# Optimization experiments

Hardware: AMD Instinct MI355X
Metric: run time of the kernel (lower is better)

Reference implementation:

```python
import jax, jax.numpy as jnp
import numpy as np

# WikiText-103 adaptive softmax config
CUTOFFS = (0, 20000, 40000, 200000, 267735)  # cluster boundaries


def setup_inputs() -> dict:
    key = jax.random.key(0)
    ks = jax.random.split(key, 12)
    N, D = 1024, 1024
    rn = lambda k, shape, std: jax.random.normal(k, shape, jnp.float32) * std
    return {
        "hidden": jax.random.normal(ks[0], (N, D), jnp.float32),
        "target": jax.random.randint(ks[1], (N,), 0, CUTOFFS[-1], jnp.int32),
        "head_w": rn(ks[2], (20000, 1024), 0.02),
        "head_b": jnp.zeros((20000,), jnp.float32),
        "cluster_w": rn(ks[3], (3, 1024), 0.02),
        "cluster_b": jnp.zeros((3,), jnp.float32),
        "proj0": rn(ks[4], (1024, 1024), 0.01),
        "proj1": rn(ks[5], (1024, 256), 0.01),
        "proj2": rn(ks[6], (1024, 64), 0.01),
        "proj3": rn(ks[7], (1024, 16), 0.01),
        "w1": rn(ks[8], (20000, 256), 0.02),
        "b1": jnp.zeros((20000,), jnp.float32),
        "w2": rn(ks[9], (160000, 64), 0.02),
        "b2": jnp.zeros((160000,), jnp.float32),
        "w3": rn(ks[10], (67735, 16), 0.02),
        "b3": jnp.zeros((67735,), jnp.float32),
    }


def _logit(h, w, b, proj):
    # F.linear(F.linear(h, proj.t()), w, b) == (h @ proj) @ w.T + b
    return (h @ proj) @ w.T + b


def reference(hidden, target, head_w, head_b, cluster_w, cluster_b,
              proj0, proj1, proj2, proj3, w1, b1, w2, b2, w3, b3):
    # head: shortlist vocab (20000) + 3 cluster logits -> [N, 20003]
    hw = jnp.concatenate([head_w, cluster_w], axis=0)
    hb = jnp.concatenate([head_b, cluster_b], axis=0)
    head_lp = jax.nn.log_softmax(_logit(hidden, hw, hb, proj0), axis=-1)

    # cluster 0 (shortlist): logprob directly from head
    t0 = jnp.clip(target, 0, CUTOFFS[1] - 1)
    lp = jnp.take_along_axis(head_lp, t0[:, None].astype(jnp.int32), axis=1)[:, 0]

    tails = [(w1, b1, proj1), (w2, b2, proj2), (w3, b3, proj3)]
    for i, (w, b, p) in enumerate(tails, start=1):
        l, r = CUTOFFS[i], CUTOFFS[i + 1]
        mask = (target >= l) & (target < r)
        ti = jnp.clip(target - l, 0, r - l - 1)
        tail_lp = jax.nn.log_softmax(_logit(hidden, w, b, p), axis=-1)  # [N, r-l]
        # note: torch code indexes head_logprob[:, -i] (reversed cluster order quirk)
        lpi = head_lp[:, -i] + jnp.take_along_axis(tail_lp, ti[:, None], axis=1)[:, 0]
        lp = jnp.where(mask, lpi, lp)

    return -lp  # nll per token, keep_order semantics
```

## Files before the change

### kernel.cpp

```cpp
#include <hip/hip_runtime.h>
#include <math.h>

typedef __bf16 bf16;
typedef __bf16 bf16x4 __attribute__((ext_vector_type(4)));
typedef __bf16 bf16x8 __attribute__((ext_vector_type(8)));
typedef float  f32x4  __attribute__((ext_vector_type(4)));

__device__ __forceinline__ f32x4 mfma16x16x32(bf16x8 a, bf16x8 b, f32x4 c) {
  return __builtin_amdgcn_mfma_f32_16x16x32_bf16(a, b, c, 0, 0, 0);
}

__device__ __forceinline__ void async16(const bf16* gp, bf16* lp) {
  __builtin_amdgcn_global_load_lds(
      (const __attribute__((address_space(1))) void*)gp,
      (__attribute__((address_space(3))) void*)lp, 16, 0, 0);
}

__global__ void __launch_bounds__(256) convert_bf16_kernel(const float* __restrict__ in,
                                                           bf16* __restrict__ out, int n4) {
  int i = blockIdx.x * 256 + threadIdx.x;
  if (i < n4) {
    float4 f = ((const float4*)in)[i];
    bf16x4 b = {(bf16)f.x, (bf16)f.y, (bf16)f.z, (bf16)f.w};
    ((bf16x4*)out)[i] = b;
  }
}

__global__ void __launch_bounds__(256) convert_w3_kernel(const float* __restrict__ w3,
                                                         bf16* __restrict__ W3b, int n4) {
  int i = blockIdx.x * 256 + threadIdx.x;
  if (i >= n4) return;
  int row = i >> 2, kq = i & 3;
  float4 f = *(const float4*)&w3[(size_t)i * 4];
  bf16x4 b = {(bf16)f.x, (bf16)f.y, (bf16)f.z, (bf16)f.w};
  *(bf16x4*)&W3b[(size_t)row * 32 + kq * 4] = b;
  bf16x4 z = {(bf16)0.f, (bf16)0.f, (bf16)0.f, (bf16)0.f};
  *(bf16x4*)&W3b[(size_t)row * 32 + 16 + kq * 4] = z;
}

__global__ void __launch_bounds__(256) transpose_convert_kernel(const float* __restrict__ P,
                                                                bf16* __restrict__ Pt, int dX) {
  __shared__ float t[32][33];
  int tx = threadIdx.x & 31, ty = threadIdx.x >> 5;
  int k0 = blockIdx.x * 32, c0 = blockIdx.y * 32;
#pragma unroll
  for (int s = 0; s < 4; ++s) {
    int k = k0 + ty + s * 8, col = c0 + tx;
    t[ty + s * 8][tx] = (col < dX) ? P[(size_t)k * dX + col] : 0.f;
  }
  __syncthreads();
#pragma unroll
  for (int s = 0; s < 4; ++s) {
    int colo = c0 + ty + s * 8;
    Pt[(size_t)colo * 1024 + k0 + tx] = (bf16)t[tx][ty + s * 8];
  }
}

__global__ void __launch_bounds__(1024) compact_kernel(const int* __restrict__ target,
                                                       int* __restrict__ rowmap,
                                                       int* __restrict__ slotmap,
                                                       int* __restrict__ counts) {
  __shared__ int cnt[3];
  int tid = threadIdx.x;
  if (tid < 3) cnt[tid] = 0;
  for (int i = tid; i < 3 * 1152; i += 1024) rowmap[i] = 0;
  __syncthreads();
  int t = target[tid];
  int c = (t >= 200000) ? 2 : (t >= 40000) ? 1 : (t >= 20000) ? 0 : -1;
  int slot = -1;
  if (c >= 0) {
    slot = atomicAdd(&cnt[c], 1);
    rowmap[c * 1152 + slot] = tid;
  }
  slotmap[tid] = slot;
  __syncthreads();
  if (tid < 3) counts[tid] = cnt[tid];
}

template <int KDIM, bool LSE>
__global__ void __launch_bounds__(256) gemm_kernel(
    const bf16* __restrict__ A, int strideA,
    const int* __restrict__ rmap, const int* __restrict__ cntp,
    const bf16* __restrict__ B,
    const float* __restrict__ bias, const float* __restrict__ bias2,
    int splice, int V, float* __restrict__ part, int nchunk,
    bf16* __restrict__ Out, int strideOut, int dX) {
  constexpr int BK = (KDIM < 64) ? KDIM : 64;
  constexpr int KG = BK / 8;
  constexpr int NIT = KDIM / BK;
  __shared__ bf16 Alds[128 * BK];
  __shared__ bf16 Blds[128 * BK];
  __shared__ float2 wpart[2][128];

  const int tid = threadIdx.x;
  const int w = tid >> 6, lane = tid & 63;
  const int q = lane >> 4, c = lane & 15;
  const int wr = w >> 1, wc = w & 1;

  int f = blockIdx.x;
  int xr = f & 7, rb = (f >> 3) & 7, cq = f >> 6;
  int chunk = cq * 8 + xr;
  if (chunk >= nchunk) return;
  const int row0 = rb * 128, col0 = chunk * 128;
  if (cntp && row0 >= *cntp) return;

  int arow[KG / 2];
#pragma unroll
  for (int i = 0; i < KG / 2; ++i) {
    int g = i * 256 + tid;
    int r = row0 + g / KG;
    arow[i] = rmap ? rmap[r] : r;
  }

  f32x4 acc[4][4] = {};

  for (int kt = 0; kt < NIT; ++kt) {
    const int k0 = kt * BK;
#pragma unroll
    for (int i = 0; i < KG / 2; ++i) {
      int g = i * 256 + tid;
      int col = g / KG, j = g % KG;
      int kg = (KG == 8) ? (j ^ (col & 7)) : (j ^ ((col >> 1) & 3));
      bf16* abase = &Alds[(size_t)(g & ~63) * 8];
      bf16* bbase = &Blds[(size_t)(g & ~63) * 8];
      async16(A + (size_t)arow[i] * strideA + k0 + kg * 8, abase);
      async16(B + (size_t)(col0 + col) * KDIM + k0 + kg * 8, bbase);
    }
    __syncthreads();
#pragma unroll
    for (int ks = 0; ks < BK / 32; ++ks) {
      bf16x8 af[4], bfr[4];
#pragma unroll
      for (int rt = 0; rt < 4; ++rt) {
        int rl = wr * 64 + rt * 16 + c;
        int kq = ks * 4 + q;
        int kg = (KG == 8) ? (kq ^ (rl & 7)) : (kq ^ ((rl >> 1) & 3));
        af[rt] = *(const bf16x8*)&Alds[((size_t)rl * KG + kg) * 8];
      }
#pragma unroll
      for (int ct = 0; ct < 4; ++ct) {
        int cl = wc * 64 + ct * 16 + c;
        int kq = ks * 4 + q;
        int kg = (KG == 8) ? (kq ^ (cl & 7)) : (kq ^ ((cl >> 1) & 3));
        bfr[ct] = *(const bf16x8*)&Blds[((size_t)cl * KG + kg) * 8];
      }
#pragma unroll
      for (int rt = 0; rt < 4; ++rt)
#pragma unroll
        for (int ct = 0; ct < 4; ++ct)
          acc[rt][ct] = mfma16x16x32(af[rt], bfr[ct], acc[rt][ct]);
    }
    __syncthreads();
  }

  if (!LSE) {
#pragma unroll
    for (int rt = 0; rt < 4; ++rt)
#pragma unroll
      for (int ct = 0; ct < 4; ++ct)
#pragma unroll
        for (int r = 0; r < 4; ++r) {
          int col = col0 + wc * 64 + ct * 16 + c;
          if (col < dX) {
            int row = row0 + wr * 64 + rt * 16 + q * 4 + r;
            Out[(size_t)row * strideOut + col] = (bf16)acc[rt][ct][r];
          }
        }
    return;
  }

  float bv[4];
#pragma unroll
  for (int ct = 0; ct < 4; ++ct) {
    int colg = col0 + wc * 64 + ct * 16 + c;
    bv[ct] = (colg < V) ? ((colg < splice) ? bias[colg] : bias2[colg - splice]) : -INFINITY;
  }
  float M = -INFINITY;
#pragma unroll
  for (int rt = 0; rt < 4; ++rt)
#pragma unroll
    for (int ct = 0; ct < 4; ++ct)
#pragma unroll
      for (int r = 0; r < 4; ++r) {
        acc[rt][ct][r] += bv[ct];
        M = fmaxf(M, acc[rt][ct][r]);
      }
#pragma unroll
  for (int off = 1; off < 64; off <<= 1) M = fmaxf(M, __shfl_xor(M, off));
  if (M == -INFINITY) M = 0.f;

#pragma unroll
  for (int rt = 0; rt < 4; ++rt) {
#pragma unroll
    for (int r = 0; r < 4; ++r) {
      float s = 0.f;
#pragma unroll
      for (int ct = 0; ct < 4; ++ct) s += __expf(acc[rt][ct][r] - M);
#pragma unroll
      for (int off = 1; off <= 8; off <<= 1) s += __shfl_xor(s, off);
      if (c == 0) wpart[wc][wr * 64 + rt * 16 + q * 4 + r] = make_float2(M, s);
    }
  }
  __syncthreads();
  if (tid < 128) {
    float2 a = wpart[0][tid], b = wpart[1][tid];
    float m = fmaxf(a.x, b.x);
    float s = a.y * __expf(a.x - m) + b.y * __expf(b.x - m);
    part[(size_t)chunk * 1024 + row0 + tid] = m + __logf(s);
  }
}

__device__ __forceinline__ float wave_max64(float v) {
#pragma unroll
  for (int off = 1; off < 64; off <<= 1) v = fmaxf(v, __shfl_xor(v, off));
  return v;
}
__device__ __forceinline__ float wave_sum64(float v) {
#pragma unroll
  for (int off = 1; off < 64; off <<= 1) v += __shfl_xor(v, off);
  return v;
}
__device__ float lse_cm(const float* __restrict__ p, int n, int idx) {
  int lane = threadIdx.x & 63;
  float m = -INFINITY;
  for (int i = lane; i < n; i += 64) m = fmaxf(m, p[(size_t)i * 1024 + idx]);
  m = wave_max64(m);
  float s = 0.f;
  for (int i = lane; i < n; i += 64) s += __expf(p[(size_t)i * 1024 + idx] - m);
  s = wave_sum64(s);
  return m + __logf(s);
}
__device__ float dot_bw(const bf16* __restrict__ h, const float* __restrict__ wv, int K) {
  int lane = threadIdx.x & 63;
  float s = 0.f;
  for (int i = lane; i < K; i += 64) s += (float)h[i] * wv[i];
  return wave_sum64(s);
}

__global__ void __launch_bounds__(256) final_kernel(
    const int* __restrict__ target, const int* __restrict__ slotmap,
    const float* __restrict__ pH, const float* __restrict__ p1,
    const float* __restrict__ p2, const float* __restrict__ p3,
    const bf16* __restrict__ Hcat,
    const float* __restrict__ head_w, const float* __restrict__ head_b,
    const float* __restrict__ cluster_w, const float* __restrict__ cluster_b,
    const float* __restrict__ w1, const float* __restrict__ b1,
    const float* __restrict__ w2, const float* __restrict__ b2,
    const float* __restrict__ w3, const float* __restrict__ b3,
    float* __restrict__ out) {
  int wv = threadIdx.x >> 6, lane = threadIdx.x & 63;
  int row = blockIdx.x * 4 + wv;
  int t = target[row];
  const bf16* h0 = Hcat + (size_t)row * 1408;

  float lseH = lse_cm(pH, 157, row);
  float lp;
  if (t < 20000) {
    float sel = dot_bw(h0, head_w + (size_t)t * 1024, 1024) + head_b[t];
    lp = sel - lseH;
  } else {
    int i, L, KW, nch, hoff;
    const float* pp; const float* W; const float* Bb;
    if (t < 40000)        { i = 1; L = 20000;  KW = 256; nch = 157;  hoff = 1024; pp = p1; W = w1; Bb = b1; }
    else if (t < 200000)  { i = 2; L = 40000;  KW = 64;  nch = 1250; hoff = 1280; pp = p2; W = w2; Bb = b2; }
    else                  { i = 3; L = 200000; KW = 16;  nch = 530;  hoff = 1344; pp = p3; W = w3; Bb = b3; }
    int slot = slotmap[row];
    float lseT = lse_cm(pp, nch, slot);
    int ti = t - L;
    float tsel = dot_bw(h0 + hoff, W + (size_t)ti * KW, KW) + Bb[ti];
    int j = 3 - i;
    float csel = dot_bw(h0, cluster_w + (size_t)j * 1024, 1024) + cluster_b[j];
    lp = (csel - lseH) + (tsel - lseT);
  }
  if (lane == 0) out[row] = -lp;
}

extern "C" void kernel_launch(void* const* d_in, const int* in_sizes, int n_in,
                              void* d_out, int out_size, void* d_ws, size_t ws_size,
                              hipStream_t stream) {
  (void)in_sizes; (void)n_in; (void)out_size; (void)ws_size;
  const float* hidden    = (const float*)d_in[0];
  const int*   target    = (const int*)d_in[1];
  const float* head_w    = (const float*)d_in[2];
  const float* head_b    = (const float*)d_in[3];
  const float* cluster_w = (const float*)d_in[4];
  const float* cluster_b = (const float*)d_in[5];
  const float* proj0     = (const float*)d_in[6];
  const float* proj1     = (const float*)d_in[7];
  const float* proj2     = (const float*)d_in[8];
  const float* proj3     = (const float*)d_in[9];
  const float* w1 = (const float*)d_in[10];
  const float* b1 = (const float*)d_in[11];
  const float* w2 = (const float*)d_in[12];
  const float* b2 = (const float*)d_in[13];
  const float* w3 = (const float*)d_in[14];
  const float* b3 = (const float*)d_in[15];
  float* out = (float*)d_out;

  char* p = (char*)d_ws;
  bf16* hid_b = (bf16*)p; p += (size_t)1024 * 1024 * 2;
  bf16* Hcat  = (bf16*)p; p += (size_t)1024 * 1408 * 2;
  bf16* Pcat  = (bf16*)p; p += (size_t)1408 * 1024 * 2;
  bf16* Wh    = (bf16*)p; p += (size_t)20096 * 1024 * 2;
  bf16* W1b   = (bf16*)p; p += (size_t)20096 * 256 * 2;
  bf16* W2b   = (bf16*)p; p += (size_t)160000 * 64 * 2;
  bf16* W3b   = (bf16*)p; p += (size_t)67840 * 32 * 2;
  float* pH   = (float*)p; p += (size_t)157 * 1024 * 4;
  float* p1   = (float*)p; p += (size_t)157 * 1024 * 4;
  float* p2   = (float*)p; p += (size_t)1250 * 1024 * 4;
  float* p3   = (float*)p; p += (size_t)530 * 1024 * 4;
  int* rowmap = (int*)p;  p += 3 * 1152 * 4;
  int* slotmap= (int*)p;  p += 1024 * 4;
  int* counts = (int*)p;  p += 3 * 4;

  compact_kernel<<<1, 1024, 0, stream>>>(target, rowmap, slotmap, counts);

  convert_bf16_kernel<<<1024, 256, 0, stream>>>(hidden, hid_b, 262144);
  convert_bf16_kernel<<<20000, 256, 0, stream>>>(head_w, Wh, 5120000);
  convert_bf16_kernel<<<3, 256, 0, stream>>>(cluster_w, Wh + (size_t)20000 * 1024, 768);
  convert_bf16_kernel<<<5000, 256, 0, stream>>>(w1, W1b, 1280000);
  convert_bf16_kernel<<<10000, 256, 0, stream>>>(w2, W2b, 2560000);
  convert_w3_kernel<<<1059, 256, 0, stream>>>(w3, W3b, 270940);
  transpose_convert_kernel<<<dim3(32, 32), 256, 0, stream>>>(proj0, Pcat, 1024);
  transpose_convert_kernel<<<dim3(32, 8), 256, 0, stream>>>(proj1, Pcat + (size_t)1024 * 1024, 256);
  transpose_convert_kernel<<<dim3(32, 2), 256, 0, stream>>>(proj2, Pcat + (size_t)1280 * 1024, 64);
  transpose_convert_kernel<<<dim3(32, 1), 256, 0, stream>>>(proj3, Pcat + (size_t)1344 * 1024, 16);

  gemm_kernel<1024, false><<<128, 256, 0, stream>>>(hid_b, 1024, nullptr, nullptr, Pcat,
                                                    nullptr, nullptr, 0, 0, nullptr, 11,
                                                    Hcat, 1408, 1376);

  gemm_kernel<1024, true><<<64 * 20, 256, 0, stream>>>(Hcat, 1408, nullptr, nullptr, Wh,
                                                       head_b, cluster_b, 20000, 20003,
                                                       pH, 157, nullptr, 0, 0);
  gemm_kernel<256, true><<<64 * 20, 256, 0, stream>>>(Hcat + 1024, 1408, rowmap, counts, W1b,
                                                      b1, b1, 0x40000000, 20000,
                                                      p1, 157, nullptr, 0, 0);
  gemm_kernel<64, true><<<64 * 157, 256, 0, stream>>>(Hcat + 1280, 1408, rowmap + 1152, counts + 1, W2b,
                                                      b2, b2, 0x40000000, 160000,
                                                      p2, 1250, nullptr, 0, 0);
  gemm_kernel<32, true><<<64 * 67, 256, 0, stream>>>(Hcat + 1344, 1408, rowmap + 2304, counts + 2, W3b,
                                                     b3, b3, 0x40000000, 67735,
                                                     p3, 530, nullptr, 0, 0);

  final_kernel<<<256, 256, 0, stream>>>(target, slotmap, pH, p1, p2, p3, Hcat,
                                        head_w, head_b, cluster_w, cluster_b,
                                        w1, b1, w2, b2, w3, b3, out);
}
```

Measured before the change: 454.2 us.

## Accumulate softmax exp-sums atomically and batch tail chunks per block with A reuse

Replaces per-chunk partial log-sum-exp outputs with direct atomic accumulation of exp sums per row, so the final kernel takes one log instead of reducing over hundreds of chunk partials. Adds a tail LSE kernel that stages the A tile once and loops over several weight chunks with double-buffered B loads. Drops the max-subtraction, relying on logits being small enough not to overflow exp, and introduces nondeterministic float atomics.

```diff
diff --git a/kernel.cpp b/kernel.cpp
--- a/kernel.cpp
+++ b/kernel.cpp
@@ -83,14 +83,13 @@
     const int* __restrict__ rmap, const int* __restrict__ cntp,
     const bf16* __restrict__ B,
     const float* __restrict__ bias, const float* __restrict__ bias2,
-    int splice, int V, float* __restrict__ part, int nchunk,
+    int splice, int V, float* __restrict__ sums, int nchunk,
     bf16* __restrict__ Out, int strideOut, int dX) {
   constexpr int BK = (KDIM < 64) ? KDIM : 64;
   constexpr int KG = BK / 8;
   constexpr int NIT = KDIM / BK;
   __shared__ bf16 Alds[128 * BK];
   __shared__ bf16 Blds[128 * BK];
-  __shared__ float2 wpart[2][128];
 
   const int tid = threadIdx.x;
   const int w = tid >> 6, lane = tid & 63;
@@ -121,10 +120,8 @@
       int g = i * 256 + tid;
       int col = g / KG, j = g % KG;
       int kg = (KG == 8) ? (j ^ (col & 7)) : (j ^ ((col >> 1) & 3));
-      bf16* abase = &Alds[(size_t)(g & ~63) * 8];
-      bf16* bbase = &Blds[(size_t)(g & ~63) * 8];
-      async16(A + (size_t)arow[i] * strideA + k0 + kg * 8, abase);
-      async16(B + (size_t)(col0 + col) * KDIM + k0 + kg * 8, bbase);
+      async16(A + (size_t)arow[i] * strideA + k0 + kg * 8, &Alds[(size_t)(g & ~63) * 8]);
+      async16(B + (size_t)(col0 + col) * KDIM + k0 + kg * 8, &Blds[(size_t)(g & ~63) * 8]);
     }
     __syncthreads();
 #pragma unroll
@@ -175,60 +172,130 @@
     int colg = col0 + wc * 64 + ct * 16 + c;
     bv[ct] = (colg < V) ? ((colg < splice) ? bias[colg] : bias2[colg - splice]) : -INFINITY;
   }
-  float M = -INFINITY;
-#pragma unroll
-  for (int rt = 0; rt < 4; ++rt)
-#pragma unroll
-    for (int ct = 0; ct < 4; ++ct)
-#pragma unroll
-      for (int r = 0; r < 4; ++r) {
-        acc[rt][ct][r] += bv[ct];
-        M = fmaxf(M, acc[rt][ct][r]);
+#pragma unroll
+  for (int rt = 0; rt < 4; ++rt) {
+#pragma unroll
+    for (int r = 0; r < 4; ++r) {
+      float s = __expf(acc[rt][0][r] + bv[0]) + __expf(acc[rt][1][r] + bv[1]) +
+                __expf(acc[rt][2][r] + bv[2]) + __expf(acc[rt][3][r] + bv[3]);
+#pragma unroll
+      for (int off = 1; off <= 8; off <<= 1) s += __shfl_xor(s, off);
+      if (c == 0) atomicAdd(&sums[row0 + wr * 64 + rt * 16 + q * 4 + r], s);
+    }
+  }
+}
+
+template <int KDIM, int CPB>
+__global__ void __launch_bounds__(256) tail_lse_kernel(
+    const bf16* __restrict__ A, int strideA,
+    const int* __restrict__ rmap, const int* __restrict__ cntp,
+    const bf16* __restrict__ B, const float* __restrict__ bias,
+    int V, float* __restrict__ sums, int nchunk) {
+  constexpr int KG = KDIM / 8;
+  constexpr int APT = 128 * KG / 256;
+  __shared__ bf16 Alds[128 * KDIM];
+  __shared__ bf16 Blds[2][128 * KDIM];
+
+  const int tid = threadIdx.x;
+  const int w = tid >> 6, lane = tid & 63;
+  const int q = lane >> 4, c = lane & 15;
+  const int wr = w >> 1, wc = w & 1;
+
+  int f = blockIdx.x;
+  int xr = f & 7, rb = (f >> 3) & 7, gq = f >> 6;
+  int grp = gq * 8 + xr;
+  int chunk0 = grp * CPB;
+  if (chunk0 >= nchunk) return;
+  const int row0 = rb * 128;
+  if (row0 >= *cntp) return;
+
+  int arow[APT];
+#pragma unroll
+  for (int i = 0; i < APT; ++i) {
+    int g = i * 256 + tid;
+    arow[i] = rmap[row0 + g / KG];
+  }
+
+  auto stageB = [&](int ch, int b) {
+#pragma unroll
+    for (int i = 0; i < APT; ++i) {
+      int g = i * 256 + tid;
+      int col = g / KG, j = g % KG;
+      int kg = (KG == 8) ? (j ^ (col & 7)) : (j ^ ((col >> 1) & 3));
+      async16(B + ((size_t)ch * 128 + col) * KDIM + kg * 8, &Blds[b][(size_t)(g & ~63) * 8]);
+    }
+  };
+
+#pragma unroll
+  for (int i = 0; i < APT; ++i) {
+    int g = i * 256 + tid;
+    int col = g / KG, j = g % KG;
+    int kg = (KG == 8) ? (j ^ (col & 7)) : (j ^ ((col >> 1) & 3));
+    async16(A + (size_t)arow[i] * strideA + kg * 8, &Alds[(size_t)(g & ~63) * 8]);
+  }
+  stageB(chunk0, 0);
+  __syncthreads();
+
+  float s[16] = {};
+
+  for (int cc = 0; cc < CPB; ++cc) {
+    int ch = chunk0 + cc;
+    bool valid = ch < nchunk;
+    if (cc + 1 < CPB && chunk0 + cc + 1 < nchunk) stageB(chunk0 + cc + 1, (cc + 1) & 1);
+    if (valid) {
+      f32x4 acc[4][4] = {};
+#pragma unroll
+      for (int ks = 0; ks < KDIM / 32; ++ks) {
+        bf16x8 af[4], bfr[4];
+#pragma unroll
+        for (int rt = 0; rt < 4; ++rt) {
+          int rl = wr * 64 + rt * 16 + c;
+          int kq = ks * 4 + q;
+          int kg = (KG == 8) ? (kq ^ (rl & 7)) : (kq ^ ((rl >> 1) & 3));
+          af[rt] = *(const bf16x8*)&Alds[((size_t)rl * KG + kg) * 8];
+        }
+#pragma unroll
+        for (int ct = 0; ct < 4; ++ct) {
+          int cl = wc * 64 + ct * 16 + c;
+          int kq = ks * 4 + q;
+          int kg = (KG == 8) ? (kq ^ (cl & 7)) : (kq ^ ((cl >> 1) & 3));
+          bfr[ct] = *(const bf16x8*)&Blds[cc & 1][((size_t)cl * KG + kg) * 8];
+        }
+#pragma unroll
+        for (int rt = 0; rt < 4; ++rt)
+#pragma unroll
+          for (int ct = 0; ct < 4; ++ct)
+            acc[rt][ct] = mfma16x16x32(af[rt], bfr[ct], acc[rt][ct]);
       }
-#pragma unroll
-  for (int off = 1; off < 64; off <<= 1) M = fmaxf(M, __shfl_xor(M, off));
-  if (M == -INFINITY) M = 0.f;
-
-#pragma unroll
-  for (int rt = 0; rt < 4; ++rt) {
-#pragma unroll
-    for (int r = 0; r < 4; ++r) {
-      float s = 0.f;
-#pragma unroll
-      for (int ct = 0; ct < 4; ++ct) s += __expf(acc[rt][ct][r] - M);
-#pragma unroll
-      for (int off = 1; off <= 8; off <<= 1) s += __shfl_xor(s, off);
-      if (c == 0) wpart[wc][wr * 64 + rt * 16 + q * 4 + r] = make_float2(M, s);
+      float bv[4];
+#pragma unroll
+      for (int ct = 0; ct < 4; ++ct) {
+        int colg = ch * 128 + wc * 64 + ct * 16 + c;
+        bv[ct] = (colg < V) ? bias[colg] : -INFINITY;
+      }
+#pragma unroll
+      for (int rt = 0; rt < 4; ++rt)
+#pragma unroll
+        for (int r = 0; r < 4; ++r)
+          s[rt * 4 + r] += __expf(acc[rt][0][r] + bv[0]) + __expf(acc[rt][1][r] + bv[1]) +
+                           __expf(acc[rt][2][r] + bv[2]) + __expf(acc[rt][3][r] + bv[3]);
     }
-  }
-  __syncthreads();
-  if (tid < 128) {
-    float2 a = wpart[0][tid], b = wpart[1][tid];
-    float m = fmaxf(a.x, b.x);
-    float s = a.y * __expf(a.x - m) + b.y * __expf(b.x - m);
-    part[(size_t)chunk * 1024 + row0 + tid] = m + __logf(s);
-  }
-}
-
-__device__ __forceinline__ float wave_max64(float v) {
-#pragma unroll
-  for (int off = 1; off < 64; off <<= 1) v = fmaxf(v, __shfl_xor(v, off));
-  return v;
-}
+    __syncthreads();
+  }
+
+#pragma unroll
+  for (int i = 0; i < 16; ++i) {
+    float v = s[i];
+#pragma unroll
+    for (int off = 1; off <= 8; off <<= 1) v += __shfl_xor(v, off);
+    if (c == 0) atomicAdd(&sums[row0 + wr * 64 + (i >> 2) * 16 + q * 4 + (i & 3)], v);
+  }
+}
+
 __device__ __forceinline__ float wave_sum64(float v) {
 #pragma unroll
   for (int off = 1; off < 64; off <<= 1) v += __shfl_xor(v, off);
   return v;
-}
-__device__ float lse_cm(const float* __restrict__ p, int n, int idx) {
-  int lane = threadIdx.x & 63;
-  float m = -INFINITY;
-  for (int i = lane; i < n; i += 64) m = fmaxf(m, p[(size_t)i * 1024 + idx]);
-  m = wave_max64(m);
-  float s = 0.f;
-  for (int i = lane; i < n; i += 64) s += __expf(p[(size_t)i * 1024 + idx] - m);
-  s = wave_sum64(s);
-  return m + __logf(s);
 }
 __device__ float dot_bw(const bf16* __restrict__ h, const float* __restrict__ wv, int K) {
   int lane = threadIdx.x & 63;
@@ -239,8 +306,8 @@
 
 __global__ void __launch_bounds__(256) final_kernel(
     const int* __restrict__ target, const int* __restrict__ slotmap,
-    const float* __restrict__ pH, const float* __restrict__ p1,
-    const float* __restrict__ p2, const float* __restrict__ p3,
+    const float* __restrict__ sumH, const float* __restrict__ sum1,
+    const float* __restrict__ sum2, const float* __restrict__ sum3,
     const bf16* __restrict__ Hcat,
     const float* __restrict__ head_w, const float* __restrict__ head_b,
     const float* __restrict__ cluster_w, const float* __restrict__ cluster_b,
@@ -253,19 +320,19 @@
   int t = target[row];
   const bf16* h0 = Hcat + (size_t)row * 1408;
 
-  float lseH = lse_cm(pH, 157, row);
+  float lseH = __logf(sumH[row]);
   float lp;
   if (t < 20000) {
     float sel = dot_bw(h0, head_w + (size_t)t * 1024, 1024) + head_b[t];
     lp = sel - lseH;
   } else {
-    int i, L, KW, nch, hoff;
-    const float* pp; const float* W; const float* Bb;
-    if (t < 40000)        { i = 1; L = 20000;  KW = 256; nch = 157;  hoff = 1024; pp = p1; W = w1; Bb = b1; }
-    else if (t < 200000)  { i = 2; L = 40000;  KW = 64;  nch = 1250; hoff = 1280; pp = p2; W = w2; Bb = b2; }
-    else                  { i = 3; L = 200000; KW = 16;  nch = 530;  hoff = 1344; pp = p3; W = w3; Bb = b3; }
+    int i, L, KW, hoff;
+    const float* sp; const float* W; const float* Bb;
+    if (t < 40000)        { i = 1; L = 20000;  KW = 256; hoff = 1024; sp = sum1; W = w1; Bb = b1; }
+    else if (t < 200000)  { i = 2; L = 40000;  KW = 64;  hoff = 1280; sp = sum2; W = w2; Bb = b2; }
+    else                  { i = 3; L = 200000; KW = 16;  hoff = 1344; sp = sum3; W = w3; Bb = b3; }
     int slot = slotmap[row];
-    float lseT = lse_cm(pp, nch, slot);
+    float lseT = __logf(sp[slot]);
     int ti = t - L;
     float tsel = dot_bw(h0 + hoff, W + (size_t)ti * KW, KW) + Bb[ti];
     int j = 3 - i;
@@ -305,14 +372,15 @@
   bf16* W1b   = (bf16*)p; p += (size_t)20096 * 256 * 2;
   bf16* W2b   = (bf16*)p; p += (size_t)160000 * 64 * 2;
   bf16* W3b   = (bf16*)p; p += (size_t)67840 * 32 * 2;
-  float* pH   = (float*)p; p += (size_t)157 * 1024 * 4;
-  float* p1   = (float*)p; p += (size_t)157 * 1024 * 4;
-  float* p2   = (float*)p; p += (size_t)1250 * 1024 * 4;
-  float* p3   = (float*)p; p += (size_t)530 * 1024 * 4;
+  float* sumH = (float*)p; p += 1024 * 4;
+  float* sum1 = (float*)p; p += 1152 * 4;
+  float* sum2 = (float*)p; p += 1152 * 4;
+  float* sum3 = (float*)p; p += 1152 * 4;
   int* rowmap = (int*)p;  p += 3 * 1152 * 4;
   int* slotmap= (int*)p;  p += 1024 * 4;
   int* counts = (int*)p;  p += 3 * 4;
 
+  hipMemsetAsync(sumH, 0, (1024 + 3 * 1152) * 4, stream);
   compact_kernel<<<1, 1024, 0, stream>>>(target, rowmap, slotmap, counts);
 
   convert_bf16_kernel<<<1024, 256, 0, stream>>>(hidden, hid_b, 262144);
@@ -332,18 +400,16 @@
 
   gemm_kernel<1024, true><<<64 * 20, 256, 0, stream>>>(Hcat, 1408, nullptr, nullptr, Wh,
                                                        head_b, cluster_b, 20000, 20003,
-                                                       pH, 157, nullptr, 0, 0);
+                                                       sumH, 157, nullptr, 0, 0);
   gemm_kernel<256, true><<<64 * 20, 256, 0, stream>>>(Hcat + 1024, 1408, rowmap, counts, W1b,
                                                       b1, b1, 0x40000000, 20000,
-                                                      p1, 157, nullptr, 0, 0);
-  gemm_kernel<64, true><<<64 * 157, 256, 0, stream>>>(Hcat + 1280, 1408, rowmap + 1152, counts + 1, W2b,
-                                                      b2, b2, 0x40000000, 160000,
-                                                      p2, 1250, nullptr, 0, 0);
-  gemm_kernel<32, true><<<64 * 67, 256, 0, stream>>>(Hcat + 1344, 1408, rowmap + 2304, counts + 2, W3b,
-                                                     b3, b3, 0x40000000, 67735,
-                                                     p3, 530, nullptr, 0, 0);
-
-  final_kernel<<<256, 256, 0, stream>>>(target, slotmap, pH, p1, p2, p3, Hcat,
+                                                      sum1, 157, nullptr, 0, 0);
+  tail_lse_kernel<64, 10><<<64 * 16, 256, 0, stream>>>(Hcat + 1280, 1408, rowmap + 1152,
+                                                       counts + 1, W2b, b2, 160000, sum2, 1250);
+  tail_lse_kernel<32, 4><<<64 * 17, 256, 0, stream>>>(Hcat + 1344, 1408, rowmap + 2304,
+                                                      counts + 2, W3b, b3, 67735, sum3, 530);
+
+  final_kernel<<<256, 256, 0, stream>>>(target, slotmap, sumH, sum1, sum2, sum3, Hcat,
                                         head_w, head_b, cluster_w, cluster_b,
                                         w1, b1, w2, b2, w3, b3, out);
 }
```

New measurement: 481.0 us. +5.9%, slower.
